# Kernel optimization log

Measured on AMD Instinct MI355X. Metric: run time of the kernel, lower is better.

The kernel has to match this reference:

```python
import jax, jax.numpy as jnp
import numpy as np

N_ROI = 116; G = 128; DEG = 32
N = G * N_ROI          # 14848 nodes
E = G * N_ROI * DEG    # 475136 edges
HID = 64; HEADS = 4; HC = HEADS * HID  # 256
EDIM = 5; EMB = 16; NG = 8; OUT = 2
NEG = 0.01      # nn.LeakyReLU default slope
NEG_ATT = 0.2   # GATv2 internal negative_slope
EPS = 1e-5


def leaky(x, s=NEG):
    return jnp.where(x >= 0, x, s * x)


def seg_softmax(logits, seg, n):
    # numerically stable softmax over edges grouped by target node
    m = jax.ops.segment_max(logits, seg, num_segments=n)
    m = jnp.where(jnp.isfinite(m), m, 0.0)
    ex = jnp.exp(logits - m[seg])
    s = jax.ops.segment_sum(ex, seg, num_segments=n)
    return ex / (s[seg] + 1e-16)


def _xav(k, shape):
    return jax.random.normal(k, shape, jnp.float32) * np.sqrt(2.0 / sum(shape)).astype(np.float32)


def setup_inputs() -> dict:
    key = jax.random.key(0)
    ks = jax.random.split(key, 40)
    x = jax.random.normal(ks[0], (N, N_ROI), jnp.float32)
    off = (jnp.arange(G, dtype=jnp.int32) * N_ROI)[:, None]
    src = (jax.random.randint(ks[1], (G, N_ROI * DEG), 0, N_ROI, jnp.int32) + off).reshape(-1)
    dst = (jax.random.randint(ks[2], (G, N_ROI * DEG), 0, N_ROI, jnp.int32) + off).reshape(-1)
    edge_index = jnp.stack([src, dst])  # [2, E], block-diagonal per graph
    edge_attr = jax.random.normal(ks[3], (E, EDIM), jnp.float32)
    grp = np.repeat(np.arange(NG, dtype=np.int32), [15] * 7 + [11])  # partition of 116 ROIs
    node_group = jnp.tile(jnp.asarray(grp), G)
    batch = jnp.repeat(jnp.arange(G, dtype=jnp.int32), N_ROI)
    p = {
        'group_emb': _xav(ks[4], (NG, EMB)),
        'W_embed': _xav(ks[5], (N_ROI + EMB, HID)), 'b_embed': jnp.zeros((HID,), jnp.float32),
        'We_enc': _xav(ks[6], (EDIM, HID)), 'be_enc': jnp.zeros((HID,), jnp.float32),
        'W1': _xav(ks[7], (HID, HID)), 'b1': jnp.zeros((HID,), jnp.float32),
        'W2': _xav(ks[8], (HID, HID)), 'b2': jnp.zeros((HID,), jnp.float32),
        'ln_g': jnp.ones((HID,), jnp.float32), 'ln_b': jnp.zeros((HID,), jnp.float32),
        'l0_Wl': _xav(ks[9], (HID, HC)), 'l0_Wr': _xav(ks[10], (HID, HC)),
        'l0_We': _xav(ks[11], (EDIM, HC)), 'l0_att': _xav(ks[12], (HEADS, HID)),
        'l0_b': jnp.zeros((HC,), jnp.float32),
        'l0_bn_g': jnp.ones((HC,), jnp.float32), 'l0_bn_b': jnp.zeros((HC,), jnp.float32),
        'l1_Wl': _xav(ks[13], (HC, HC)), 'l1_Wr': _xav(ks[14], (HC, HC)),
        'l1_We': _xav(ks[15], (EDIM, HC)), 'l1_att': _xav(ks[16], (HEADS, HID)),
        'l1_b': jnp.zeros((HC,), jnp.float32),
        'l1_bn_g': jnp.ones((HC,), jnp.float32), 'l1_bn_b': jnp.zeros((HC,), jnp.float32),
        'fc2_W': _xav(ks[17], (HC, OUT)), 'fc2_b': jnp.zeros((OUT,), jnp.float32),
    }
    return dict(x=x, edge_index=edge_index, edge_attr=edge_attr, batch=batch, node_group=node_group, **p)


def _gat_layer(h, src, dst, edge_attr, Wl, Wr, We, att, b, bn_g, bn_b):
    n = h.shape[0]
    xl = (h @ Wl).reshape(n, HEADS, HID)
    xr = (h @ Wr).reshape(n, HEADS, HID)
    e = (edge_attr @ We).reshape(-1, HEADS, HID)
    xls = xl[src]                                   # [E,H,C]
    z = leaky(xls + xr[dst] + e, NEG_ATT)
    logits = jnp.einsum('ehc,hc->eh', z, att)       # GATv2 attention scores
    alpha = seg_softmax(logits, dst, n)             # softmax over incoming edges per node
    out = jax.ops.segment_sum(xls * alpha[:, :, None], dst, num_segments=n)
    out = out.reshape(n, HC) + b
    mu = out.mean(0); var = ((out - mu) ** 2).mean(0)  # BatchNorm (batch stats)
    out = (out - mu) / jnp.sqrt(var + EPS) * bn_g + bn_b
    return leaky(out)


def reference(x, edge_index, edge_attr, batch, node_group, group_emb, W_embed, b_embed,
              We_enc, be_enc, W1, b1, W2, b2, ln_g, ln_b,
              l0_Wl, l0_Wr, l0_We, l0_att, l0_b, l0_bn_g, l0_bn_b,
              l1_Wl, l1_Wr, l1_We, l1_att, l1_b, l1_bn_g, l1_bn_b, fc2_W, fc2_b):
    src, dst = edge_index[0], edge_index[1]
    # BrainEncodeEmbed: group embedding concat + projection
    h = jnp.concatenate([x, group_emb[node_group]], axis=-1)   # [N, 132]
    h = leaky(h @ W_embed + b_embed)                            # [N, HID]
    eemb = leaky(edge_attr @ We_enc + be_enc)                   # [E, HID]
    # GINEConv: sum_j ReLU(x_j + e_ij), eps=0, then MLP
    msg = jax.nn.relu(h[src] + eemb)
    h = h + jax.ops.segment_sum(msg, dst, num_segments=N)
    h = leaky(h @ W1 + b1) @ W2 + b2
    h = leaky(h)
    mu = h.mean(-1, keepdims=True)
    v = ((h - mu) ** 2).mean(-1, keepdims=True)
    h = (h - mu) / jnp.sqrt(v + EPS) * ln_g + ln_b              # LayerNorm
    # stacked GATv2 blocks
    h = _gat_layer(h, src, dst, edge_attr, l0_Wl, l0_Wr, l0_We, l0_att, l0_b, l0_bn_g, l0_bn_b)
    h = _gat_layer(h, src, dst, edge_attr, l1_Wl, l1_Wr, l1_We, l1_att, l1_b, l1_bn_g, l1_bn_b)
    # global mean pool + classifier
    cnt = jax.ops.segment_sum(jnp.ones((h.shape[0],), h.dtype), batch, num_segments=G)
    pooled = jax.ops.segment_sum(h, batch, num_segments=G) / cnt[:, None]
    return pooled @ fc2_W + fc2_b
```

## Files before the change

### kernel.cpp

```cpp
#include <hip/hip_runtime.h>
#include <hip/hip_bf16.h>

#define NN     14848
#define NE     475136
#define NROI   116
#define NGRAPH 128
#define EPG    3712
#define HID    64
#define HC     256
#define NEG    0.01f
#define NEGA   0.2f
#define EPB    2304
#define XPADB  66

typedef __attribute__((ext_vector_type(8))) short short8;
typedef __attribute__((ext_vector_type(4))) float floatx4;
typedef __attribute__((ext_vector_type(2))) float floatx2;

__device__ __forceinline__ float leaky(float x, float s) { return fmaxf(x, s * x); }

__device__ __forceinline__ short f2bf(float f) {
    unsigned u = __float_as_uint(f);
    unsigned r = (u + 0x7fffu + ((u >> 16) & 1u)) >> 16;
    return (short)r;
}
__device__ __forceinline__ float bf2f(unsigned short b) {
    return __uint_as_float((unsigned)b << 16);
}

__global__ __launch_bounds__(256) void k_front(
    const float* __restrict__ x, const int* __restrict__ ng,
    const float* __restrict__ gemb, const float* __restrict__ W,
    const float* __restrict__ b, float* __restrict__ h0,
    const int* __restrict__ src, const int* __restrict__ dst,
    const float* __restrict__ ea,
    int* __restrict__ row_start, int* __restrict__ row_cnt,
    int* __restrict__ ssd, float* __restrict__ ea_s,
    float* __restrict__ stats01,
    const float* __restrict__ Wl0, const float* __restrict__ Wr0,
    const float* __restrict__ Wl1, const float* __restrict__ Wr1,
    short* __restrict__ Wt0, short* __restrict__ Wt1)
{
    const int tid = threadIdx.x;
    if (blockIdx.x < NN / 4) {
        const int w = tid >> 6, c = tid & 63;
        const int n = blockIdx.x * 4 + w;
        __shared__ float in[4][132];
        for (int k = c; k < NROI; k += 64) in[w][k] = x[n * NROI + k];
        if (c < 16) in[w][NROI + c] = gemb[ng[n] * 16 + c];
        __syncthreads();
        float acc = b[c];
        #pragma unroll 4
        for (int k = 0; k < 132; k++) acc = fmaf(in[w][k], W[k * 64 + c], acc);
        h0[n * 64 + c] = leaky(acc, NEG);
    } else if (blockIdx.x < NN / 4 + NGRAPH) {
        const int g = blockIdx.x - NN / 4;
        if (g < 2) {
            for (int i = tid; i < 512; i += 256) stats01[g * 512 + i] = 0.f;
        }
        const int e0 = g * EPG, nb = g * NROI;
        __shared__ int cnt[NROI], start[NROI], cur[NROI];
        if (tid < NROI) cnt[tid] = 0;
        __syncthreads();
        for (int i = tid; i < EPG; i += 256) atomicAdd(&cnt[dst[e0 + i] - nb], 1);
        __syncthreads();
        if (tid == 0) {
            int s = 0;
            for (int r = 0; r < NROI; r++) { start[r] = s; s += cnt[r]; }
        }
        __syncthreads();
        if (tid < NROI) {
            row_start[nb + tid] = e0 + start[tid];
            row_cnt[nb + tid] = cnt[tid];
            cur[tid] = start[tid];
        }
        __syncthreads();
        for (int i = tid; i < EPG; i += 256) {
            const int e = e0 + i, dl = dst[e] - nb;
            const int pos = atomicAdd(&cur[dl], 1);
            const int gi = e0 + pos;
            ssd[gi] = (src[e] - nb) | (dl << 16);
            const float4 q = make_float4(ea[e * 5], ea[e * 5 + 1], ea[e * 5 + 2], ea[e * 5 + 3]);
            *(float4*)&ea_s[(size_t)gi * 8] = q;
            ea_s[(size_t)gi * 8 + 4] = ea[e * 5 + 4];
        }
    } else {
        const int bb = blockIdx.x - (NN / 4 + NGRAPH);
        if (bb < 512) {
            const int n = bb;
            for (int k = tid; k < 64; k += 256) {
                const float v = (n < 256) ? Wl0[k * 256 + n] : Wr0[k * 256 + (n - 256)];
                Wt0[(size_t)n * 64 + k] = f2bf(v);
            }
        } else {
            const int n = bb - 512;
            for (int k = tid; k < 256; k += 256) {
                const float v = (n < 256) ? Wl1[k * 256 + n] : Wr1[k * 256 + (n - 256)];
                Wt1[(size_t)n * 256 + k] = f2bf(v);
            }
        }
    }
}

__global__ __launch_bounds__(256) void k_gine_mlp_ln(
    const float* __restrict__ h0, const int* __restrict__ row_start,
    const int* __restrict__ row_cnt, const int* __restrict__ ssd,
    const float* __restrict__ ea_s,
    const float* __restrict__ We, const float* __restrict__ be,
    const float* __restrict__ W1, const float* __restrict__ b1,
    const float* __restrict__ W2, const float* __restrict__ b2,
    const float* __restrict__ lg_, const float* __restrict__ lb_,
    short* __restrict__ hn)
{
    const int tid = threadIdx.x, w = tid >> 6, lane = tid & 63;
    const int row = blockIdx.x * 4 + w;
    const int nb = (row / NROI) * NROI;
    const int st = row_start[row], cnt = row_cnt[row];
    const float w0 = We[lane], w1 = We[64 + lane], w2 = We[128 + lane],
                w3 = We[192 + lane], w4 = We[256 + lane];
    const float bec = be[lane];
    float g0 = 0.f, g1 = 0.f, g2 = 0.f, g3 = 0.f;
    int j = 0;
    for (; j + 4 <= cnt; j += 4) {
        const int i0 = st + j, i1 = st + j + 1, i2 = st + j + 2, i3 = st + j + 3;
        const int s0 = nb + (ssd[i0] & 0xffff), s1 = nb + (ssd[i1] & 0xffff),
                  s2 = nb + (ssd[i2] & 0xffff), s3 = nb + (ssd[i3] & 0xffff);
        const float h_0 = h0[s0 * 64 + lane], h_1 = h0[s1 * 64 + lane],
                    h_2 = h0[s2 * 64 + lane], h_3 = h0[s3 * 64 + lane];
        const float4 qa = *(const float4*)&ea_s[(size_t)i0 * 8];
        const float qa4 = ea_s[(size_t)i0 * 8 + 4];
        const float4 qb = *(const float4*)&ea_s[(size_t)i1 * 8];
        const float qb4 = ea_s[(size_t)i1 * 8 + 4];
        const float4 qc = *(const float4*)&ea_s[(size_t)i2 * 8];
        const float qc4 = ea_s[(size_t)i2 * 8 + 4];
        const float4 qd = *(const float4*)&ea_s[(size_t)i3 * 8];
        const float qd4 = ea_s[(size_t)i3 * 8 + 4];
        float e0_ = bec, e1_ = bec, e2_ = bec, e3_ = bec;
        e0_ = fmaf(qa.x, w0, e0_); e1_ = fmaf(qb.x, w0, e1_);
        e2_ = fmaf(qc.x, w0, e2_); e3_ = fmaf(qd.x, w0, e3_);
        e0_ = fmaf(qa.y, w1, e0_); e1_ = fmaf(qb.y, w1, e1_);
        e2_ = fmaf(qc.y, w1, e2_); e3_ = fmaf(qd.y, w1, e3_);
        e0_ = fmaf(qa.z, w2, e0_); e1_ = fmaf(qb.z, w2, e1_);
        e2_ = fmaf(qc.z, w2, e2_); e3_ = fmaf(qd.z, w2, e3_);
        e0_ = fmaf(qa.w, w3, e0_); e1_ = fmaf(qb.w, w3, e1_);
        e2_ = fmaf(qc.w, w3, e2_); e3_ = fmaf(qd.w, w3, e3_);
        e0_ = fmaf(qa4, w4, e0_);  e1_ = fmaf(qb4, w4, e1_);
        e2_ = fmaf(qc4, w4, e2_);  e3_ = fmaf(qd4, w4, e3_);
        g0 += fmaxf(h_0 + leaky(e0_, NEG), 0.f);
        g1 += fmaxf(h_1 + leaky(e1_, NEG), 0.f);
        g2 += fmaxf(h_2 + leaky(e2_, NEG), 0.f);
        g3 += fmaxf(h_3 + leaky(e3_, NEG), 0.f);
    }
    for (; j < cnt; j++) {
        const int idx = st + j;
        const int s = nb + (ssd[idx] & 0xffff);
        const float4 q = *(const float4*)&ea_s[(size_t)idx * 8];
        const float q4 = ea_s[(size_t)idx * 8 + 4];
        float em = bec;
        em = fmaf(q.x, w0, em); em = fmaf(q.y, w1, em); em = fmaf(q.z, w2, em);
        em = fmaf(q.w, w3, em); em = fmaf(q4, w4, em);
        g0 += fmaxf(h0[s * 64 + lane] + leaky(em, NEG), 0.f);
    }
    const float aggv = (g0 + g1) + (g2 + g3);
    __shared__ float v[4][64], t[4][64];
    v[w][lane] = h0[row * 64 + lane] + aggv;
    __syncthreads();
    float a = b1[lane];
    #pragma unroll 8
    for (int k = 0; k < 64; k++) a = fmaf(v[w][k], W1[k * 64 + lane], a);
    t[w][lane] = leaky(a, NEG);
    __syncthreads();
    float o = b2[lane];
    #pragma unroll 8
    for (int k = 0; k < 64; k++) o = fmaf(t[w][k], W2[k * 64 + lane], o);
    o = leaky(o, NEG);
    float s = o;
    #pragma unroll
    for (int off = 32; off; off >>= 1) s += __shfl_xor(s, off);
    const float mu = s * (1.f / 64.f);
    const float d = o - mu;
    float s2 = d * d;
    #pragma unroll
    for (int off = 32; off; off >>= 1) s2 += __shfl_xor(s2, off);
    hn[row * 64 + lane] = f2bf(d * rsqrtf(s2 * (1.f / 64.f) + 1e-5f) * lg_[lane] + lb_[lane]);
}

template <int D, bool BN>
__global__ __launch_bounds__(256) void k_gemm(
    const short* __restrict__ A, const float* __restrict__ Vin,
    const float* __restrict__ stats, const float* __restrict__ bn_g,
    const float* __restrict__ bn_b,
    const short* __restrict__ Wt,
    float* __restrict__ X, float* __restrict__ Y)
{
    const int m0 = blockIdx.x * 16;
    const int w = threadIdx.x >> 6, lane = threadIdx.x & 63;
    const int n0 = w * 128;
    const int r = lane & 15, q = lane >> 4;
    __shared__ float sc_s[256], sh_s[256];
    if constexpr (BN) {
        const int c = threadIdx.x;
        const float inv_n = 1.f / (float)NN;
        const float mu = stats[c] * inv_n;
        float var = stats[256 + c] * inv_n - mu * mu;
        var = fmaxf(var, 0.f);
        const float rsg = rsqrtf(var + 1e-5f) * bn_g[c];
        sc_s[c] = rsg;
        sh_s[c] = bn_b[c] - mu * rsg;
        __syncthreads();
    }
    floatx4 acc[8];
    #pragma unroll
    for (int t = 0; t < 8; t++) acc[t] = (floatx4){0.f, 0.f, 0.f, 0.f};
    const short* Arow = A + (size_t)(m0 + r) * D + q * 8;
    const float* Vrow = Vin + (size_t)(m0 + r) * D + q * 8;
    const short* Brow = Wt + (size_t)(n0 + r) * D + q * 8;
    #pragma unroll
    for (int k0 = 0; k0 < D; k0 += 32) {
        short8 a;
        if constexpr (BN) {
            const float4 v0 = *(const float4*)(Vrow + k0);
            const float4 v1 = *(const float4*)(Vrow + k0 + 4);
            const int cb = q * 8 + k0;
            a[0] = f2bf(leaky(fmaf(v0.x, sc_s[cb + 0], sh_s[cb + 0]), NEG));
            a[1] = f2bf(leaky(fmaf(v0.y, sc_s[cb + 1], sh_s[cb + 1]), NEG));
            a[2] = f2bf(leaky(fmaf(v0.z, sc_s[cb + 2], sh_s[cb + 2]), NEG));
            a[3] = f2bf(leaky(fmaf(v0.w, sc_s[cb + 3], sh_s[cb + 3]), NEG));
            a[4] = f2bf(leaky(fmaf(v1.x, sc_s[cb + 4], sh_s[cb + 4]), NEG));
            a[5] = f2bf(leaky(fmaf(v1.y, sc_s[cb + 5], sh_s[cb + 5]), NEG));
            a[6] = f2bf(leaky(fmaf(v1.z, sc_s[cb + 6], sh_s[cb + 6]), NEG));
            a[7] = f2bf(leaky(fmaf(v1.w, sc_s[cb + 7], sh_s[cb + 7]), NEG));
        } else {
            a = *(const short8*)(Arow + k0);
        }
        #pragma unroll
        for (int t = 0; t < 8; t++) {
            const short8 b = *(const short8*)(Brow + (size_t)t * 16 * D + k0);
            acc[t] = __builtin_amdgcn_mfma_f32_16x16x32_bf16(a, b, acc[t], 0, 0, 0);
        }
    }
    #pragma unroll
    for (int t = 0; t < 8; t++) {
        const int ncol = n0 + t * 16 + r;
        #pragma unroll
        for (int g2 = 0; g2 < 4; g2++) {
            const int row = m0 + q * 4 + g2;
            if (ncol < 256) X[(size_t)row * HC + ncol] = acc[t][g2];
            else            Y[(size_t)row * HC + (ncol - 256)] = acc[t][g2];
        }
    }
}

__global__ __launch_bounds__(256, 6) void k_gat(
    const int* __restrict__ row_start, const int* __restrict__ row_cnt,
    const int* __restrict__ ssd, const float* __restrict__ ea_s,
    const float* __restrict__ We, const float* __restrict__ att,
    const float* __restrict__ bias,
    const float* __restrict__ X, const float* __restrict__ Y,
    float* __restrict__ V, float* __restrict__ stats)
{
    const int g = blockIdx.x & 127;
    const int sub = blockIdx.x >> 7;
    const int h = sub >> 1;
    const int half = sub & 1;
    const int tid = threadIdx.x, w = tid >> 6, lane = tid & 63;
    const int nb = g * NROI, e0 = g * EPG, hc = h * 64;
    const int r0 = half * 58, r1 = r0 + 58;
    const int es = row_start[nb + r0];
    const int ee = (r1 < NROI) ? row_start[nb + r1] : e0 + EPG;

    __shared__ short Xs[NROI * XPADB];
    __shared__ float lg[EPB];
    __shared__ float inv_s[58];

    for (int r = w; r < NROI; r += 4)
        Xs[r * XPADB + lane] = f2bf(X[(size_t)(nb + r) * HC + hc + lane]);
    __syncthreads();

    const int ne = ee - es;
    for (int i = tid; i < ne; i += 256) {
        const int e = es + i;
        const int sd = ssd[e];
        const int sl = sd & 0xffff, dl = sd >> 16;
        const float4 q = *(const float4*)&ea_s[(size_t)e * 8];
        const float q4 = ea_s[(size_t)e * 8 + 4];
        const floatx2 qx = {q.x, q.x}, qy = {q.y, q.y}, qz = {q.z, q.z},
                      qw = {q.w, q.w}, qv = {q4, q4};
        const float* yrow = &Y[(size_t)(nb + dl) * HC + hc];
        const unsigned* xrow = (const unsigned*)&Xs[sl * XPADB];
        floatx2 lacc = {0.f, 0.f};
        #pragma unroll 8
        for (int c = 0; c < 64; c += 2) {
            const floatx2 y2 = *(const floatx2*)(yrow + c);
            const unsigned xp = xrow[c >> 1];
            const floatx2 xs2 = {__uint_as_float(xp << 16),
                                 __uint_as_float(xp & 0xffff0000u)};
            const floatx2 w0 = *(const floatx2*)(We + 0 * HC + hc + c);
            const floatx2 w1 = *(const floatx2*)(We + 1 * HC + hc + c);
            const floatx2 w2 = *(const floatx2*)(We + 2 * HC + hc + c);
            const floatx2 w3 = *(const floatx2*)(We + 3 * HC + hc + c);
            const floatx2 w4 = *(const floatx2*)(We + 4 * HC + hc + c);
            floatx2 ep = qx * w0;
            ep += qy * w1;
            ep += qz * w2;
            ep += qw * w3;
            ep += qv * w4;
            const floatx2 z = xs2 + y2 + ep;
            const floatx2 zs = z * (floatx2){NEGA, NEGA};
            const floatx2 lk = {fmaxf(z.x, zs.x), fmaxf(z.y, zs.y)};
            const floatx2 a2 = *(const floatx2*)(att + hc + c);
            lacc += a2 * lk;
        }
        lg[i] = lacc.x + lacc.y;
    }
    __syncthreads();

    for (int r = r0 + w; r < r1; r += 4) {
        const int stl = row_start[nb + r] - es;
        const int cnt = row_cnt[nb + r];
        float m = -INFINITY;
        for (int j = lane; j < cnt; j += 64) m = fmaxf(m, lg[stl + j]);
        #pragma unroll
        for (int off = 32; off; off >>= 1) m = fmaxf(m, __shfl_xor(m, off));
        float s = 0.f;
        for (int j = lane; j < cnt; j += 64) {
            const float e_ = __expf(lg[stl + j] - m);
            lg[stl + j] = e_;
            s += e_;
        }
        #pragma unroll
        for (int off = 32; off; off >>= 1) s += __shfl_xor(s, off);
        if (lane == 0) inv_s[r - r0] = 1.f / (s + 1e-16f);
    }
    __syncthreads();

    float ps = 0.f, ps2 = 0.f;
    const float bb = bias[hc + lane];
    for (int r = r0 + w; r < r1; r += 4) {
        const int st = row_start[nb + r];
        const int cnt = row_cnt[nb + r];
        const int stl = st - es;
        float a0 = 0.f, a1 = 0.f, a2 = 0.f, a3 = 0.f;
        int j = 0;
        for (; j + 4 <= cnt; j += 4) {
            const int s0 = ssd[st + j] & 0xffff, s1 = ssd[st + j + 1] & 0xffff,
                      s2 = ssd[st + j + 2] & 0xffff, s3 = ssd[st + j + 3] & 0xffff;
            a0 = fmaf(bf2f((unsigned short)Xs[s0 * XPADB + lane]), lg[stl + j], a0);
            a1 = fmaf(bf2f((unsigned short)Xs[s1 * XPADB + lane]), lg[stl + j + 1], a1);
            a2 = fmaf(bf2f((unsigned short)Xs[s2 * XPADB + lane]), lg[stl + j + 2], a2);
            a3 = fmaf(bf2f((unsigned short)Xs[s3 * XPADB + lane]), lg[stl + j + 3], a3);
        }
        for (; j < cnt; j++)
            a0 = fmaf(bf2f((unsigned short)Xs[(ssd[st + j] & 0xffff) * XPADB + lane]),
                      lg[stl + j], a0);
        const float vv = ((a0 + a1) + (a2 + a3)) * inv_s[r - r0] + bb;
        V[(size_t)(nb + r) * HC + hc + lane] = vv;
        ps += vv;
        ps2 += vv * vv;
    }
    __syncthreads();
    lg[tid] = ps;
    lg[256 + tid] = ps2;
    __syncthreads();
    if (tid < 64) {
        float s1 = 0.f, s2 = 0.f;
        #pragma unroll
        for (int w2 = 0; w2 < 4; w2++) {
            s1 += lg[w2 * 64 + tid];
            s2 += lg[256 + w2 * 64 + tid];
        }
        atomicAdd(&stats[hc + tid], s1);
        atomicAdd(&stats[256 + hc + tid], s2);
    }
}

__global__ __launch_bounds__(256) void k_pool_fc(
    const float* __restrict__ V, const float* __restrict__ stats,
    const float* __restrict__ bg, const float* __restrict__ bb,
    const float* __restrict__ fW, const float* __restrict__ fb,
    float* __restrict__ out)
{
    const int g = blockIdx.x, c = threadIdx.x;
    const float inv_n = 1.f / (float)NN;
    const float mu = stats[c] * inv_n;
    float var = stats[256 + c] * inv_n - mu * mu;
    var = fmaxf(var, 0.f);
    const float rsg = rsqrtf(var + 1e-5f) * bg[c];
    const float bbc = bb[c];
    float s = 0.f;
    for (int r = 0; r < NROI; r++) {
        const float vv = (V[(size_t)(g * NROI + r) * HC + c] - mu) * rsg + bbc;
        s += leaky(vv, NEG);
    }
    s *= (1.f / (float)NROI);
    __shared__ float red[256];
    for (int o = 0; o < 2; o++) {
        red[c] = s * fW[c * 2 + o];
        __syncthreads();
        for (int off = 128; off; off >>= 1) {
            if (c < off) red[c] += red[c + off];
            __syncthreads();
        }
        if (c == 0) out[g * 2 + o] = red[0] + fb[o];
        __syncthreads();
    }
}

extern "C" void kernel_launch(void* const* d_in, const int* in_sizes, int n_in,
                              void* d_out, int out_size, void* d_ws, size_t ws_size,
                              hipStream_t stream) {
    const float* x         = (const float*)d_in[0];
    const int*   edge_idx  = (const int*)d_in[1];
    const float* edge_attr = (const float*)d_in[2];
    const int*   node_grp  = (const int*)d_in[4];
    const float* group_emb = (const float*)d_in[5];
    const float* W_embed   = (const float*)d_in[6];
    const float* b_embed   = (const float*)d_in[7];
    const float* We_enc    = (const float*)d_in[8];
    const float* be_enc    = (const float*)d_in[9];
    const float* W1        = (const float*)d_in[10];
    const float* b1        = (const float*)d_in[11];
    const float* W2        = (const float*)d_in[12];
    const float* b2        = (const float*)d_in[13];
    const float* ln_g      = (const float*)d_in[14];
    const float* ln_b      = (const float*)d_in[15];
    const float* l0_Wl     = (const float*)d_in[16];
    const float* l0_Wr     = (const float*)d_in[17];
    const float* l0_We     = (const float*)d_in[18];
    const float* l0_att    = (const float*)d_in[19];
    const float* l0_b      = (const float*)d_in[20];
    const float* l0_bn_g   = (const float*)d_in[21];
    const float* l0_bn_b   = (const float*)d_in[22];
    const float* l1_Wl     = (const float*)d_in[23];
    const float* l1_Wr     = (const float*)d_in[24];
    const float* l1_We     = (const float*)d_in[25];
    const float* l1_att    = (const float*)d_in[26];
    const float* l1_b      = (const float*)d_in[27];
    const float* l1_bn_g   = (const float*)d_in[28];
    const float* l1_bn_b   = (const float*)d_in[29];
    const float* fc2_W     = (const float*)d_in[30];
    const float* fc2_b     = (const float*)d_in[31];

    const int* src = edge_idx;
    const int* dst = edge_idx + NE;

    float* ws     = (float*)d_ws;
    float* h0     = ws;
    float* X      = h0 + (size_t)64 * NN;
    float* Y      = X + (size_t)HC * NN;
    float* V      = Y + (size_t)HC * NN;
    float* stats0 = V + (size_t)HC * NN;
    float* stats1 = stats0 + 512;
    float* ea_s   = stats1 + 512;
    int* row_start = (int*)(ea_s + (size_t)8 * NE);
    int* row_cnt   = row_start + NN;
    int* ssd       = row_cnt + NN;
    short* hn_b    = (short*)(ssd + NE);
    short* Wt0     = hn_b + (size_t)64 * NN;
    short* Wt1     = Wt0 + 512 * 64;

    float* out = (float*)d_out;

    k_front<<<NN / 4 + NGRAPH + 1024, 256, 0, stream>>>(
        x, node_grp, group_emb, W_embed, b_embed, h0,
        src, dst, edge_attr, row_start, row_cnt, ssd, ea_s, stats0,
        l0_Wl, l0_Wr, l1_Wl, l1_Wr, Wt0, Wt1);
    k_gine_mlp_ln<<<NN / 4, 256, 0, stream>>>(h0, row_start, row_cnt, ssd, ea_s,
                                              We_enc, be_enc, W1, b1, W2, b2, ln_g, ln_b, hn_b);

    k_gemm<64, false><<<NN / 16, 256, 0, stream>>>(hn_b, nullptr, nullptr, nullptr, nullptr,
                                                   Wt0, X, Y);
    k_gat<<<NGRAPH * 8, 256, 0, stream>>>(row_start, row_cnt, ssd, ea_s,
                                          l0_We, l0_att, l0_b, X, Y, V, stats0);

    k_gemm<256, true><<<NN / 16, 256, 0, stream>>>(nullptr, V, stats0, l0_bn_g, l0_bn_b,
                                                   Wt1, X, Y);
    k_gat<<<NGRAPH * 8, 256, 0, stream>>>(row_start, row_cnt, ssd, ea_s,
                                          l1_We, l1_att, l1_b, X, Y, V, stats1);

    k_pool_fc<<<NGRAPH, 256, 0, stream>>>(V, stats1, l1_bn_g, l1_bn_b, fc2_W, fc2_b, out);
}
```

Measured before the change: 425.6 us.

## Split GAT blocks into row quarters and parallelize CSR build with prefix scan

New measurement: 427.7 us. About the same (+0.5%).

```diff
diff --git a/kernel.cpp b/kernel.cpp
--- a/kernel.cpp
+++ b/kernel.cpp
@@ -10,7 +10,7 @@
 #define HC     256
 #define NEG    0.01f
 #define NEGA   0.2f
-#define EPB    2304
+#define EPB    1312
 #define XPADB  66
 
 typedef __attribute__((ext_vector_type(8))) short short8;
@@ -42,9 +42,50 @@
     short* __restrict__ Wt0, short* __restrict__ Wt1)
 {
     const int tid = threadIdx.x;
-    if (blockIdx.x < NN / 4) {
+    if (blockIdx.x < NGRAPH) {
+        const int g = blockIdx.x;
+        if (g < 2) {
+            for (int i = tid; i < 512; i += 256) stats01[g * 512 + i] = 0.f;
+        }
+        const int e0 = g * EPG, nb = g * NROI;
+        __shared__ int cnt[NROI], start[NROI], scn[128];
+        __shared__ unsigned short pos[EPG];
+        if (tid < NROI) cnt[tid] = 0;
+        __syncthreads();
+        for (int i = tid; i < EPG; i += 256) {
+            const int dl = dst[e0 + i] - nb;
+            pos[i] = (unsigned short)atomicAdd(&cnt[dl], 1);
+        }
+        __syncthreads();
+        if (tid < 128) scn[tid] = (tid < NROI) ? cnt[tid] : 0;
+        __syncthreads();
+        #pragma unroll
+        for (int off = 1; off < 128; off <<= 1) {
+            int v = 0;
+            if (tid < 128 && tid >= off) v = scn[tid - off];
+            __syncthreads();
+            if (tid < 128) scn[tid] += v;
+            __syncthreads();
+        }
+        if (tid < NROI) {
+            const int st = scn[tid] - cnt[tid];
+            start[tid] = st;
+            row_start[nb + tid] = e0 + st;
+            row_cnt[nb + tid] = cnt[tid];
+        }
+        __syncthreads();
+        for (int i = tid; i < EPG; i += 256) {
+            const int e = e0 + i;
+            const int dl = dst[e] - nb;
+            const int gi = e0 + start[dl] + (int)pos[i];
+            ssd[gi] = (src[e] - nb) | (dl << 16);
+            const float4 q = make_float4(ea[e * 5], ea[e * 5 + 1], ea[e * 5 + 2], ea[e * 5 + 3]);
+            *(float4*)&ea_s[(size_t)gi * 8] = q;
+            ea_s[(size_t)gi * 8 + 4] = ea[e * 5 + 4];
+        }
+    } else if (blockIdx.x < NGRAPH + NN / 4) {
         const int w = tid >> 6, c = tid & 63;
-        const int n = blockIdx.x * 4 + w;
+        const int n = (blockIdx.x - NGRAPH) * 4 + w;
         __shared__ float in[4][132];
         for (int k = c; k < NROI; k += 64) in[w][k] = x[n * NROI + k];
         if (c < 16) in[w][NROI + c] = gemb[ng[n] * 16 + c];
@@ -53,39 +94,8 @@
         #pragma unroll 4
         for (int k = 0; k < 132; k++) acc = fmaf(in[w][k], W[k * 64 + c], acc);
         h0[n * 64 + c] = leaky(acc, NEG);
-    } else if (blockIdx.x < NN / 4 + NGRAPH) {
-        const int g = blockIdx.x - NN / 4;
-        if (g < 2) {
-            for (int i = tid; i < 512; i += 256) stats01[g * 512 + i] = 0.f;
-        }
-        const int e0 = g * EPG, nb = g * NROI;
-        __shared__ int cnt[NROI], start[NROI], cur[NROI];
-        if (tid < NROI) cnt[tid] = 0;
-        __syncthreads();
-        for (int i = tid; i < EPG; i += 256) atomicAdd(&cnt[dst[e0 + i] - nb], 1);
-        __syncthreads();
-        if (tid == 0) {
-            int s = 0;
-            for (int r = 0; r < NROI; r++) { start[r] = s; s += cnt[r]; }
-        }
-        __syncthreads();
-        if (tid < NROI) {
-            row_start[nb + tid] = e0 + start[tid];
-            row_cnt[nb + tid] = cnt[tid];
-            cur[tid] = start[tid];
-        }
-        __syncthreads();
-        for (int i = tid; i < EPG; i += 256) {
-            const int e = e0 + i, dl = dst[e] - nb;
-            const int pos = atomicAdd(&cur[dl], 1);
-            const int gi = e0 + pos;
-            ssd[gi] = (src[e] - nb) | (dl << 16);
-            const float4 q = make_float4(ea[e * 5], ea[e * 5 + 1], ea[e * 5 + 2], ea[e * 5 + 3]);
-            *(float4*)&ea_s[(size_t)gi * 8] = q;
-            ea_s[(size_t)gi * 8 + 4] = ea[e * 5 + 4];
-        }
     } else {
-        const int bb = blockIdx.x - (NN / 4 + NGRAPH);
+        const int bb = blockIdx.x - (NGRAPH + NN / 4);
         if (bb < 512) {
             const int n = bb;
             for (int k = tid; k < 64; k += 256) {
@@ -261,17 +271,17 @@
 {
     const int g = blockIdx.x & 127;
     const int sub = blockIdx.x >> 7;
-    const int h = sub >> 1;
-    const int half = sub & 1;
+    const int h = sub >> 2;
+    const int qtr = sub & 3;
     const int tid = threadIdx.x, w = tid >> 6, lane = tid & 63;
     const int nb = g * NROI, e0 = g * EPG, hc = h * 64;
-    const int r0 = half * 58, r1 = r0 + 58;
+    const int r0 = qtr * 29, r1 = r0 + 29;
     const int es = row_start[nb + r0];
     const int ee = (r1 < NROI) ? row_start[nb + r1] : e0 + EPG;
 
     __shared__ short Xs[NROI * XPADB];
     __shared__ float lg[EPB];
-    __shared__ float inv_s[58];
+    __shared__ float inv_s[29];
 
     for (int r = w; r < NROI; r += 4)
         Xs[r * XPADB + lane] = f2bf(X[(size_t)(nb + r) * HC + hc + lane]);
@@ -461,7 +471,7 @@
 
     float* out = (float*)d_out;
 
-    k_front<<<NN / 4 + NGRAPH + 1024, 256, 0, stream>>>(
+    k_front<<<NGRAPH + NN / 4 + 1024, 256, 0, stream>>>(
         x, node_grp, group_emb, W_embed, b_embed, h0,
         src, dst, edge_attr, row_start, row_cnt, ssd, ea_s, stats0,
         l0_Wl, l0_Wr, l1_Wl, l1_Wr, Wt0, Wt1);
@@ -470,13 +480,13 @@
 
     k_gemm<64, false><<<NN / 16, 256, 0, stream>>>(hn_b, nullptr, nullptr, nullptr, nullptr,
                                                    Wt0, X, Y);
-    k_gat<<<NGRAPH * 8, 256, 0, stream>>>(row_start, row_cnt, ssd, ea_s,
-                                          l0_We, l0_att, l0_b, X, Y, V, stats0);
+    k_gat<<<NGRAPH * 16, 256, 0, stream>>>(row_start, row_cnt, ssd, ea_s,
+                                           l0_We, l0_att, l0_b, X, Y, V, stats0);
 
     k_gemm<256, true><<<NN / 16, 256, 0, stream>>>(nullptr, V, stats0, l0_bn_g, l0_bn_b,
                                                    Wt1, X, Y);
-    k_gat<<<NGRAPH * 8, 256, 0, stream>>>(row_start, row_cnt, ssd, ea_s,
-                                          l1_We, l1_att, l1_b, X, Y, V, stats1);
+    k_gat<<<NGRAPH * 16, 256, 0, stream>>>(row_start, row_cnt, ssd, ea_s,
+                                           l1_We, l1_att, l1_b, X, Y, V, stats1);
 
     k_pool_fc<<<NGRAPH, 256, 0, stream>>>(V, stats1, l1_bn_g, l1_bn_b, fc2_W, fc2_b, out);
 }
```
